# Kernel optimization log

Hardware: AMD Instinct MI355X
Metric: run time of the kernel (lower is better)

## Reference

```python
import jax, jax.numpy as jnp
import numpy as np

N_LAYERS = 4
BN_EPS = 1e-5


def setup_inputs() -> dict:
    key = jax.random.key(0)
    ks = jax.random.split(key, 10)
    N, E, F, H = 50000, 600000, 128, 128
    x = jax.random.normal(ks[0], (N, F), dtype=jnp.float32)
    edge_index = jax.random.randint(ks[1], (2, E), 0, N, dtype=jnp.int64)
    s = 0.05  # small init to keep deep ReLU stack numerically tame
    return {
        "x": x,
        "edge_index": edge_index,
        # stacked params for the 4 GINConv MLPs (num_features == hidden)
        "conv_w1": jax.random.normal(ks[2], (N_LAYERS, F, H), dtype=jnp.float32) * s,
        "conv_b1": jnp.zeros((N_LAYERS, H), dtype=jnp.float32),
        "conv_gamma": jnp.ones((N_LAYERS, H), dtype=jnp.float32),
        "conv_beta": jnp.zeros((N_LAYERS, H), dtype=jnp.float32),
        "conv_w2": jax.random.normal(ks[3], (N_LAYERS, H, H), dtype=jnp.float32) * s,
        "conv_b2": jnp.zeros((N_LAYERS, H), dtype=jnp.float32),
        "fc1_w": jax.random.normal(ks[4], (H, H), dtype=jnp.float32) * s,
        "fc1_b": jnp.zeros((H,), dtype=jnp.float32),
        "fc2_w": jax.random.normal(ks[5], (H, 1), dtype=jnp.float32) * s,
        "fc2_b": jnp.zeros((1,), dtype=jnp.float32),
    }


def _batchnorm(h, gamma, beta):
    # training-mode BatchNorm1d: batch stats over the node axis, biased variance
    mean = jnp.mean(h, axis=0, keepdims=True)
    var = jnp.mean(jnp.square(h - mean), axis=0, keepdims=True)
    return (h - mean) * jax.lax.rsqrt(var + BN_EPS) * gamma + beta


def _gin_layer(x, src, dst, w1, b1, gamma, beta, w2, b2):
    n = x.shape[0]
    # GIN sum aggregation with eps=0: (1+eps)*x_i + sum_{j->i} x_j
    agg = x + jax.ops.segment_sum(x[src], dst, num_segments=n)
    h = jax.nn.relu(agg @ w1 + b1)
    h = _batchnorm(h, gamma, beta)
    return jax.nn.relu(h @ w2 + b2)


def reference(x, edge_index, conv_w1, conv_b1, conv_gamma, conv_beta,
              conv_w2, conv_b2, fc1_w, fc1_b, fc2_w, fc2_b):
    src, dst = edge_index[0], edge_index[1]
    h = x
    for l in range(N_LAYERS):
        h = _gin_layer(h, src, dst, conv_w1[l], conv_b1[l], conv_gamma[l],
                       conv_beta[l], conv_w2[l], conv_b2[l])
    h = jax.nn.relu(h @ fc1_w + fc1_b)
    return h @ fc2_w + fc2_b  # [N, 1]
```

## Files before the change

### kernel.cpp

```cpp
#include <hip/hip_runtime.h>

constexpr int FEAT = 128;

typedef __attribute__((ext_vector_type(8))) _Float16 f16x8;
typedef __attribute__((ext_vector_type(4))) float f32x4;

__device__ inline unsigned int halfpair(float a, float b) {
  unsigned short ua = __builtin_bit_cast(unsigned short, (_Float16)a);
  unsigned short ub = __builtin_bit_cast(unsigned short, (_Float16)b);
  return (unsigned int)ua | ((unsigned int)ub << 16);
}
__device__ inline unsigned short halfr(float a) {
  return __builtin_bit_cast(unsigned short, (_Float16)a);
}
__device__ inline float2 halfup(unsigned int u) {
  _Float16 lo = __builtin_bit_cast(_Float16, (unsigned short)(u & 0xffffu));
  _Float16 hi = __builtin_bit_cast(_Float16, (unsigned short)(u >> 16));
  return make_float2((float)lo, (float)hi);
}

__device__ __host__ inline int kperm(int k) {
  return ((k >> 5) << 5) + (((k >> 2) & 3) << 3) + (((k >> 4) & 1) << 2) + (k & 3);
}


__global__ void count_kernel(const int* __restrict__ dst, int* __restrict__ deg, int E) {
  int e = blockIdx.x * blockDim.x + threadIdx.x;
  if (e < E) atomicAdd(&deg[dst[e]], 1);
}

__global__ __launch_bounds__(256) void scan1_kernel(const int* __restrict__ in,
                                                    int* __restrict__ bsum, int n) {
  int base = blockIdx.x * 1024 + threadIdx.x * 4;
  int s = 0;
  if (base + 3 < n) {
    int4 v = *(const int4*)(in + base);
    s = v.x + v.y + v.z + v.w;
  } else {
#pragma unroll
    for (int j = 0; j < 4; j++)
      if (base + j < n) s += in[base + j];
  }
#pragma unroll
  for (int off = 1; off < 64; off <<= 1) s += __shfl_xor(s, off);
  __shared__ int ws[4];
  int lane = threadIdx.x & 63, wid = threadIdx.x >> 6;
  if (lane == 0) ws[wid] = s;
  __syncthreads();
  if (threadIdx.x == 0) bsum[blockIdx.x] = ws[0] + ws[1] + ws[2] + ws[3];
}

__global__ __launch_bounds__(64) void scan2_kernel(int* __restrict__ bsum, int nb) {
  int t = threadIdx.x;
  int v = (t < nb) ? bsum[t] : 0;
  int s = v;
#pragma unroll
  for (int off = 1; off < 64; off <<= 1) {
    int u = __shfl_up(s, off);
    if (t >= off) s += u;
  }
  if (t < nb) bsum[t] = s - v;
}

__global__ __launch_bounds__(256) void scan3_kernel(const int* __restrict__ in,
                                                    const int* __restrict__ boff,
                                                    int* __restrict__ out,
                                                    int* __restrict__ out2, int n) {
  int t = threadIdx.x;
  int base = blockIdx.x * 1024 + t * 4;
  int v0 = 0, v1 = 0, v2 = 0, v3 = 0;
  if (base + 3 < n) {
    int4 v = *(const int4*)(in + base);
    v0 = v.x; v1 = v.y; v2 = v.z; v3 = v.w;
  } else {
    if (base + 0 < n) v0 = in[base + 0];
    if (base + 1 < n) v1 = in[base + 1];
    if (base + 2 < n) v2 = in[base + 2];
  }
  int ts = v0 + v1 + v2 + v3;
  int s = ts;
  int lane = t & 63, wid = t >> 6;
#pragma unroll
  for (int off = 1; off < 64; off <<= 1) {
    int u = __shfl_up(s, off);
    if (lane >= off) s += u;
  }
  __shared__ int ws[4];
  if (lane == 63) ws[wid] = s;
  __syncthreads();
  int cross = 0;
#pragma unroll
  for (int i = 0; i < 4; i++)
    if (i < wid) cross += ws[i];
  int excl = boff[blockIdx.x] + cross + (s - ts);
  int o0 = excl, o1 = o0 + v0, o2 = o1 + v1, o3 = o2 + v2;
  if (base + 3 < n) {
    *(int4*)(out + base) = make_int4(o0, o1, o2, o3);
    *(int4*)(out2 + base) = make_int4(o0, o1, o2, o3);
  } else {
    if (base + 0 < n) { out[base + 0] = o0; out2[base + 0] = o0; }
    if (base + 1 < n) { out[base + 1] = o1; out2[base + 1] = o1; }
    if (base + 2 < n) { out[base + 2] = o2; out2[base + 2] = o2; }
  }
}

__global__ void fill_kernel(const int* __restrict__ src, const int* __restrict__ dst,
                            int* __restrict__ cursor, int* __restrict__ col, int E) {
  int e = blockIdx.x * blockDim.x + threadIdx.x;
  if (e < E) {
    int p = atomicAdd(&cursor[dst[e]], 1);
    col[p] = src[e];
  }
}


__global__ void convert_kernel(const float* __restrict__ x, unsigned short* __restrict__ xb,
                               int n4) {
  int idx = blockIdx.x * blockDim.x + threadIdx.x;
  if (idx >= n4) return;
  float4 v = ((const float4*)x)[idx];
  uint2 o;
  o.x = halfpair(v.x, v.y);
  o.y = halfpair(v.z, v.w);
  ((uint2*)xb)[idx] = o;
}


__global__ void wconv_kernel(const float* __restrict__ w1, const float* __restrict__ fc1w,
                             unsigned short* __restrict__ dst) {
  int idx = blockIdx.x * blockDim.x + threadIdx.x;
  if (idx >= 5 * FEAT * FEAT) return;
  int m = idx >> 14;
  int r = idx & (FEAT * FEAT - 1);
  int k = r >> 7, n = r & 127;
  float v = (m < 4) ? w1[idx] : fc1w[r];
  int p = kperm(k);
  int slot = p >> 3, e = p & 7;
  dst[m * FEAT * FEAT + n * FEAT + ((slot ^ (n & 7)) << 3) + e] = halfr(v);
}


__global__ void agg_kernel(const unsigned short* __restrict__ x, const int* __restrict__ rowptr,
                           const int* __restrict__ col, unsigned short* __restrict__ agg, int N) {
  int gid = blockIdx.x * blockDim.x + threadIdx.x;
  int wid = gid >> 6;
  int lane = threadIdx.x & 63;
  int node = wid * 4 + (lane >> 4);
  if (node >= N) return;
  int ln = lane & 15;
  const uint4* xr = (const uint4*)x;
  uint4 s = xr[(size_t)node * 16 + ln];
  float2 t0 = halfup(s.x), t1 = halfup(s.y), t2 = halfup(s.z), t3 = halfup(s.w);
  float a0 = t0.x, a1 = t0.y, a2 = t1.x, a3 = t1.y;
  float a4 = t2.x, a5 = t2.y, a6 = t3.x, a7 = t3.y;
  float b0 = 0.f, b1 = 0.f, b2 = 0.f, b3 = 0.f;
  float b4 = 0.f, b5 = 0.f, b6 = 0.f, b7 = 0.f;
  int e0 = rowptr[node], e1 = rowptr[node + 1];
  int e = e0;
  for (; e + 3 < e1; e += 4) {
    int c0 = col[e], c1 = col[e + 1], c2 = col[e + 2], c3 = col[e + 3];
    uint4 v = xr[(size_t)c0 * 16 + ln];
    uint4 u = xr[(size_t)c1 * 16 + ln];
    uint4 w = xr[(size_t)c2 * 16 + ln];
    uint4 z = xr[(size_t)c3 * 16 + ln];
    float2 f;
    f = halfup(v.x); a0 += f.x; a1 += f.y;
    f = halfup(v.y); a2 += f.x; a3 += f.y;
    f = halfup(v.z); a4 += f.x; a5 += f.y;
    f = halfup(v.w); a6 += f.x; a7 += f.y;
    f = halfup(u.x); b0 += f.x; b1 += f.y;
    f = halfup(u.y); b2 += f.x; b3 += f.y;
    f = halfup(u.z); b4 += f.x; b5 += f.y;
    f = halfup(u.w); b6 += f.x; b7 += f.y;
    f = halfup(w.x); a0 += f.x; a1 += f.y;
    f = halfup(w.y); a2 += f.x; a3 += f.y;
    f = halfup(w.z); a4 += f.x; a5 += f.y;
    f = halfup(w.w); a6 += f.x; a7 += f.y;
    f = halfup(z.x); b0 += f.x; b1 += f.y;
    f = halfup(z.y); b2 += f.x; b3 += f.y;
    f = halfup(z.z); b4 += f.x; b5 += f.y;
    f = halfup(z.w); b6 += f.x; b7 += f.y;
  }
  for (; e < e1; e++) {
    uint4 v = xr[(size_t)col[e] * 16 + ln];
    float2 f;
    f = halfup(v.x); a0 += f.x; a1 += f.y;
    f = halfup(v.y); a2 += f.x; a3 += f.y;
    f = halfup(v.z); a4 += f.x; a5 += f.y;
    f = halfup(v.w); a6 += f.x; a7 += f.y;
  }
  a0 += b0; a1 += b1; a2 += b2; a3 += b3;
  a4 += b4; a5 += b5; a6 += b6; a7 += b7;
  uint4 o;
  o.x = halfpair(a0, a1);
  o.y = halfpair(a2, a3);
  o.z = halfpair(a4, a5);
  o.w = halfpair(a6, a7);
  ((uint4*)agg)[(size_t)node * 16 + ln] = o;
}


__global__ __launch_bounds__(512, 4) void gemm_kernel(
    const unsigned short* __restrict__ A, const unsigned short* __restrict__ Wimg,
    const float* __restrict__ bias, unsigned short* __restrict__ C,
    float* __restrict__ pS, float* __restrict__ pQ, int N, int mode,
    const float* __restrict__ fc2w, const float* __restrict__ fc2b,
    float* __restrict__ outp) {
  __shared__ unsigned short Al[FEAT * FEAT];
  __shared__ unsigned short Wl[FEAT * FEAT];
  __shared__ float ls[FEAT], lq[FEAT];

  int tx = threadIdx.x;
  int row0 = blockIdx.x * FEAT;
  if (tx < FEAT) { ls[tx] = 0.f; lq[tx] = 0.f; }

#pragma unroll
  for (int i = 0; i < 4; i++) {
    int idx = tx + i * 512;
    ((uint4*)Wl)[idx] = ((const uint4*)Wimg)[idx];
  }
#pragma unroll
  for (int i = 0; i < 8; i++) {
    int idx = tx + i * 512;
    int r = idx >> 5;
    int c = idx & 31;
    uint2 v = make_uint2(0u, 0u);
    if (row0 + r < N) v = ((const uint2*)(A + (size_t)(row0 + r) * FEAT))[c];
    int k0 = c << 2;
    int p0 = ((k0 >> 5) << 5) + (((k0 >> 2) & 3) << 3) + (((k0 >> 4) & 1) << 2);
    int slot = p0 >> 3, half4 = (p0 >> 2) & 1;
    *(uint2*)&Al[r * FEAT + ((slot ^ (r & 7)) << 3) + (half4 << 2)] = v;
  }
  __syncthreads();

  int w = tx >> 6;
  int l = tx & 63;
  int llo = l & 15, lhi = l >> 4;
  int wr = (w >> 2) * 64;
  int wc = (w & 3) * 32;

  f32x4 acc[4][2];
#pragma unroll
  for (int mi = 0; mi < 4; mi++)
#pragma unroll
    for (int nj = 0; nj < 2; nj++) acc[mi][nj] = (f32x4)(0.f);

#pragma unroll
  for (int s = 0; s < 4; s++) {
    f16x8 af[4], wf[2];
#pragma unroll
    for (int mi = 0; mi < 4; mi++) {
      int row = wr + mi * 16 + llo;
      af[mi] = *(const f16x8*)&Al[row * FEAT + ((((s << 2) + lhi) ^ (row & 7)) << 3)];
    }
#pragma unroll
    for (int nj = 0; nj < 2; nj++) {
      int n = wc + nj * 16 + llo;
      wf[nj] = *(const f16x8*)&Wl[n * FEAT + ((((s << 2) + lhi) ^ (n & 7)) << 3)];
    }
#pragma unroll
    for (int mi = 0; mi < 4; mi++)
#pragma unroll
      for (int nj = 0; nj < 2; nj++)
        acc[mi][nj] = __builtin_amdgcn_mfma_f32_16x16x32_f16(wf[nj], af[mi], acc[mi][nj], 0, 0, 0);
  }

  if (mode == 2) {
    float* red = ls;
    float pr[4] = {0.f, 0.f, 0.f, 0.f};
#pragma unroll
    for (int nj = 0; nj < 2; nj++) {
      int colb = wc + nj * 16 + lhi * 4;
      float4 bb = *(const float4*)&bias[colb];
      float4 fw = *(const float4*)&fc2w[colb];
#pragma unroll
      for (int mi = 0; mi < 4; mi++) {
        f32x4 v = acc[mi][nj];
        float v0 = fmaxf(v[0] + bb.x, 0.f);
        float v1 = fmaxf(v[1] + bb.y, 0.f);
        float v2 = fmaxf(v[2] + bb.z, 0.f);
        float v3 = fmaxf(v[3] + bb.w, 0.f);
        pr[mi] += v0 * fw.x + v1 * fw.y + v2 * fw.z + v3 * fw.w;
      }
    }
#pragma unroll
    for (int mi = 0; mi < 4; mi++) {
      float r = pr[mi];
      r += __shfl_xor(r, 16);
      r += __shfl_xor(r, 32);
      if (lhi == 0) atomicAdd(&red[wr + mi * 16 + llo], r);
    }
    __syncthreads();
    if (tx < FEAT) {
      int row = row0 + tx;
      if (row < N) outp[row] = red[tx] + fc2b[0];
    }
    return;
  }

#pragma unroll
  for (int nj = 0; nj < 2; nj++) {
    int colb = wc + nj * 16 + lhi * 4;
    float4 bb = *(const float4*)&bias[colb];
    float ps[4] = {0.f, 0.f, 0.f, 0.f}, pq[4] = {0.f, 0.f, 0.f, 0.f};
#pragma unroll
    for (int mi = 0; mi < 4; mi++) {
      int row = row0 + wr + mi * 16 + llo;
      f32x4 v = acc[mi][nj];
      float v0 = fmaxf(v[0] + bb.x, 0.f);
      float v1 = fmaxf(v[1] + bb.y, 0.f);
      float v2 = fmaxf(v[2] + bb.z, 0.f);
      float v3 = fmaxf(v[3] + bb.w, 0.f);
      if (row < N) {
        *(uint2*)&C[(size_t)row * FEAT + colb] = make_uint2(halfpair(v0, v1), halfpair(v2, v3));
        ps[0] += v0; ps[1] += v1; ps[2] += v2; ps[3] += v3;
        pq[0] += v0 * v0; pq[1] += v1 * v1; pq[2] += v2 * v2; pq[3] += v3 * v3;
      }
    }
    if (mode == 1) {
#pragma unroll
      for (int r = 0; r < 4; r++) {
        float s2 = ps[r], q2 = pq[r];
#pragma unroll
        for (int off = 1; off < 16; off <<= 1) {
          s2 += __shfl_xor(s2, off);
          q2 += __shfl_xor(q2, off);
        }
        if (llo == 0) {
          atomicAdd(&ls[colb + r], s2);
          atomicAdd(&lq[colb + r], q2);
        }
      }
    }
  }
  if (mode == 1) {
    __syncthreads();
    if (tx < FEAT) {
      pS[(size_t)blockIdx.x * FEAT + tx] = ls[tx];
      pQ[(size_t)blockIdx.x * FEAT + tx] = lq[tx];
    }
  }
}


__global__ __launch_bounds__(64) void stats_kernel(
    const float* __restrict__ pS, const float* __restrict__ pQ, int nblk,
    const float* __restrict__ gamma, const float* __restrict__ beta,
    float* __restrict__ scf, float* __restrict__ shf, int N) {
  int c = blockIdx.x;
  int ln = threadIdx.x;
  float s = 0.f, q = 0.f;
  for (int b = ln; b < nblk; b += 64) {
    s += pS[(size_t)b * FEAT + c];
    q += pQ[(size_t)b * FEAT + c];
  }
#pragma unroll
  for (int off = 32; off; off >>= 1) {
    s += __shfl_xor(s, off);
    q += __shfl_xor(q, off);
  }
  if (ln == 0) {
    float invN = 1.0f / (float)N;
    float mean = s * invN;
    float var = q * invN - mean * mean;
    float rstd = rsqrtf(var + 1e-5f);
    float scale = gamma[c] * rstd;
    scf[c] = scale;
    shf[c] = beta[c] - mean * scale;
  }
}


__global__ __launch_bounds__(128) void fold2_kernel(
    const float* __restrict__ scf, const float* __restrict__ shf,
    const float* __restrict__ w2, const float* __restrict__ b2,
    unsigned short* __restrict__ w2f, float* __restrict__ b2f) {
  __shared__ float red[FEAT];
  int c = blockIdx.x;
  int k = threadIdx.x;
  float wv = w2[k * FEAT + c];
  int p = kperm(k);
  int slot = p >> 3, e = p & 7;
  w2f[c * FEAT + ((slot ^ (c & 7)) << 3) + e] = halfr(scf[k] * wv);
  red[k] = shf[k] * wv;
  __syncthreads();
#pragma unroll
  for (int off = 64; off > 0; off >>= 1) {
    if (k < off) red[k] += red[k + off];
    __syncthreads();
  }
  if (k == 0) b2f[c] = b2[c] + red[0];
}


extern "C" void kernel_launch(void* const* d_in, const int* in_sizes, int n_in,
                              void* d_out, int out_size, void* d_ws, size_t ws_size,
                              hipStream_t stream) {
  const float* x     = (const float*)d_in[0];
  const int*   ei    = (const int*)d_in[1];
  const float* w1    = (const float*)d_in[2];
  const float* b1    = (const float*)d_in[3];
  const float* gamma = (const float*)d_in[4];
  const float* beta  = (const float*)d_in[5];
  const float* w2    = (const float*)d_in[6];
  const float* b2    = (const float*)d_in[7];
  const float* fc1w  = (const float*)d_in[8];
  const float* fc1b  = (const float*)d_in[9];
  const float* fc2w  = (const float*)d_in[10];
  const float* fc2b  = (const float*)d_in[11];
  float* out = (float*)d_out;

  int N = in_sizes[0] / FEAT;
  int E = in_sizes[1] / 2;
  const int* srcI = ei;
  const int* dstI = ei + E;

  int gemmBlocks = (N + FEAT - 1) / FEAT;
  int n = N + 1;
  int nb = (n + 1023) / 1024;

  size_t Nf = (size_t)N * FEAT;
  unsigned short* H = (unsigned short*)d_ws;
  unsigned short* G = H + Nf;
  unsigned short* wimg = G + Nf;
  unsigned short* w2f = wimg + 5 * FEAT * FEAT;
  float* b2f = (float*)(w2f + FEAT * FEAT);
  float* scf = b2f + FEAT;
  float* shf = scf + FEAT;
  float* pS = shf + FEAT;
  float* pQ = pS + (size_t)gemmBlocks * FEAT;
  int* deg = (int*)(pQ + (size_t)gemmBlocks * FEAT);
  int* rowptr = deg + ((n + 3) & ~3);
  int* cursor = rowptr + ((n + 3) & ~3);
  int* bsum = cursor + ((n + 3) & ~3);
  int* col = bsum + 64;

  hipMemsetAsync(deg, 0, n * sizeof(int), stream);
  count_kernel<<<(E + 255) / 256, 256, 0, stream>>>(dstI, deg, E);
  scan1_kernel<<<nb, 256, 0, stream>>>(deg, bsum, n);
  scan2_kernel<<<1, 64, 0, stream>>>(bsum, nb);
  scan3_kernel<<<nb, 256, 0, stream>>>(deg, bsum, rowptr, cursor, n);
  fill_kernel<<<(E + 255) / 256, 256, 0, stream>>>(srcI, dstI, cursor, col, E);

  int n4 = (int)(Nf / 4);
  convert_kernel<<<(n4 + 255) / 256, 256, 0, stream>>>(x, H, n4);
  wconv_kernel<<<(5 * FEAT * FEAT + 255) / 256, 256, 0, stream>>>(w1, fc1w, wimg);

  int aggBlocks = (int)((((size_t)(N + 3) / 4) * 64 + 255) / 256);

  for (int l = 0; l < 4; l++) {
    agg_kernel<<<aggBlocks, 256, 0, stream>>>(H, rowptr, col, G, N);
    gemm_kernel<<<gemmBlocks, 512, 0, stream>>>(
        G, wimg + (size_t)l * FEAT * FEAT, b1 + (size_t)l * FEAT, G, pS, pQ, N, 1,
        nullptr, nullptr, nullptr);
    stats_kernel<<<FEAT, 64, 0, stream>>>(pS, pQ, gemmBlocks, gamma + (size_t)l * FEAT,
                                          beta + (size_t)l * FEAT, scf, shf, N);
    fold2_kernel<<<FEAT, FEAT, 0, stream>>>(scf, shf, w2 + (size_t)l * FEAT * FEAT,
                                            b2 + (size_t)l * FEAT, w2f, b2f);
    gemm_kernel<<<gemmBlocks, 512, 0, stream>>>(
        G, w2f, b2f, H, nullptr, nullptr, N, 0, nullptr, nullptr, nullptr);
  }

  gemm_kernel<<<gemmBlocks, 512, 0, stream>>>(
      H, wimg + (size_t)4 * FEAT * FEAT, fc1b, nullptr, nullptr, nullptr, N, 2,
      fc2w, fc2b, out);
}
```

Baseline: 393.3 us.

## Fuse prep kernels and read GEMM weight fragments directly from global memory

Merges the degree count, input fp16 conversion and weight-image conversion into one launch using block-range dispatch, which removes two kernel launches. In the GEMM, the weight tile is no longer staged in LDS; each wave loads its W fragments straight from global/L2, halving shared memory per block. The A-tile staging now uses 16-byte global loads instead of 8-byte ones. The trade-off is that the weight fragments, which are identical for every block, are fetched repeatedly from cache instead of once into LDS, while the smaller LDS footprint may allow more blocks per CU.

```diff
diff --git a/kernel.cpp b/kernel.cpp
--- a/kernel.cpp
+++ b/kernel.cpp
@@ -24,10 +24,38 @@
 }
 
 
-__global__ void count_kernel(const int* __restrict__ dst, int* __restrict__ deg, int E) {
-  int e = blockIdx.x * blockDim.x + threadIdx.x;
-  if (e < E) atomicAdd(&deg[dst[e]], 1);
-}
+__global__ __launch_bounds__(256) void prep_kernel(
+    const float* __restrict__ x, unsigned short* __restrict__ xb, int n4,
+    const float* __restrict__ w1, const float* __restrict__ fc1w,
+    unsigned short* __restrict__ wimg,
+    const int* __restrict__ dst, int* __restrict__ deg, int E, int B1, int B2) {
+  int bid = blockIdx.x;
+  if (bid < B1) {
+    int idx = bid * 256 + threadIdx.x;
+    if (idx < n4) {
+      float4 v = ((const float4*)x)[idx];
+      uint2 o;
+      o.x = halfpair(v.x, v.y);
+      o.y = halfpair(v.z, v.w);
+      ((uint2*)xb)[idx] = o;
+    }
+  } else if (bid < B1 + B2) {
+    int idx = (bid - B1) * 256 + threadIdx.x;
+    if (idx < 5 * FEAT * FEAT) {
+      int m = idx >> 14;
+      int r = idx & (FEAT * FEAT - 1);
+      int k = r >> 7, n = r & 127;
+      float v = (m < 4) ? w1[idx] : fc1w[r];
+      int p = kperm(k);
+      int slot = p >> 3, e = p & 7;
+      wimg[m * FEAT * FEAT + n * FEAT + ((slot ^ (n & 7)) << 3) + e] = halfr(v);
+    }
+  } else {
+    int e = (bid - B1 - B2) * 256 + threadIdx.x;
+    if (e < E) atomicAdd(&deg[dst[e]], 1);
+  }
+}
+
 
 __global__ __launch_bounds__(256) void scan1_kernel(const int* __restrict__ in,
                                                     int* __restrict__ bsum, int n) {
@@ -111,32 +139,6 @@
     int p = atomicAdd(&cursor[dst[e]], 1);
     col[p] = src[e];
   }
-}
-
-
-__global__ void convert_kernel(const float* __restrict__ x, unsigned short* __restrict__ xb,
-                               int n4) {
-  int idx = blockIdx.x * blockDim.x + threadIdx.x;
-  if (idx >= n4) return;
-  float4 v = ((const float4*)x)[idx];
-  uint2 o;
-  o.x = halfpair(v.x, v.y);
-  o.y = halfpair(v.z, v.w);
-  ((uint2*)xb)[idx] = o;
-}
-
-
-__global__ void wconv_kernel(const float* __restrict__ w1, const float* __restrict__ fc1w,
-                             unsigned short* __restrict__ dst) {
-  int idx = blockIdx.x * blockDim.x + threadIdx.x;
-  if (idx >= 5 * FEAT * FEAT) return;
-  int m = idx >> 14;
-  int r = idx & (FEAT * FEAT - 1);
-  int k = r >> 7, n = r & 127;
-  float v = (m < 4) ? w1[idx] : fc1w[r];
-  int p = kperm(k);
-  int slot = p >> 3, e = p & 7;
-  dst[m * FEAT * FEAT + n * FEAT + ((slot ^ (n & 7)) << 3) + e] = halfr(v);
 }
 
 
@@ -207,7 +209,6 @@
     const float* __restrict__ fc2w, const float* __restrict__ fc2b,
     float* __restrict__ outp) {
   __shared__ unsigned short Al[FEAT * FEAT];
-  __shared__ unsigned short Wl[FEAT * FEAT];
   __shared__ float ls[FEAT], lq[FEAT];
 
   int tx = threadIdx.x;
@@ -217,19 +218,16 @@
 #pragma unroll
   for (int i = 0; i < 4; i++) {
     int idx = tx + i * 512;
-    ((uint4*)Wl)[idx] = ((const uint4*)Wimg)[idx];
-  }
-#pragma unroll
-  for (int i = 0; i < 8; i++) {
-    int idx = tx + i * 512;
-    int r = idx >> 5;
-    int c = idx & 31;
-    uint2 v = make_uint2(0u, 0u);
-    if (row0 + r < N) v = ((const uint2*)(A + (size_t)(row0 + r) * FEAT))[c];
-    int k0 = c << 2;
-    int p0 = ((k0 >> 5) << 5) + (((k0 >> 2) & 3) << 3) + (((k0 >> 4) & 1) << 2);
-    int slot = p0 >> 3, half4 = (p0 >> 2) & 1;
-    *(uint2*)&Al[r * FEAT + ((slot ^ (r & 7)) << 3) + (half4 << 2)] = v;
+    int r = idx >> 4;
+    int c = idx & 15;
+    uint4 v = make_uint4(0u, 0u, 0u, 0u);
+    if (row0 + r < N) v = ((const uint4*)(A + (size_t)(row0 + r) * FEAT))[c];
+    int k0 = c << 3;
+    int slotA = ((k0 >> 5) << 2) + ((k0 >> 2) & 3);
+    int sub = (k0 >> 4) & 1;
+    int sw = r & 7;
+    *(uint2*)&Al[r * FEAT + ((slotA ^ sw) << 3) + (sub << 2)] = make_uint2(v.x, v.y);
+    *(uint2*)&Al[r * FEAT + (((slotA + 1) ^ sw) << 3) + (sub << 2)] = make_uint2(v.z, v.w);
   }
   __syncthreads();
 
@@ -239,6 +237,9 @@
   int wr = (w >> 2) * 64;
   int wc = (w & 3) * 32;
 
+  const unsigned short* w0p = Wimg + (size_t)(wc + llo) * FEAT;
+  int m0 = (wc + llo) & 7;
+
   f32x4 acc[4][2];
 #pragma unroll
   for (int mi = 0; mi < 4; mi++)
@@ -247,22 +248,21 @@
 
 #pragma unroll
   for (int s = 0; s < 4; s++) {
-    f16x8 af[4], wf[2];
+    int so = (s << 2) + lhi;
+    int woff = (so ^ m0) << 3;
+    f16x8 wf0 = *(const f16x8*)&w0p[woff];
+    f16x8 wf1 = *(const f16x8*)&w0p[16 * FEAT + woff];
+    f16x8 af[4];
 #pragma unroll
     for (int mi = 0; mi < 4; mi++) {
       int row = wr + mi * 16 + llo;
-      af[mi] = *(const f16x8*)&Al[row * FEAT + ((((s << 2) + lhi) ^ (row & 7)) << 3)];
-    }
-#pragma unroll
-    for (int nj = 0; nj < 2; nj++) {
-      int n = wc + nj * 16 + llo;
-      wf[nj] = *(const f16x8*)&Wl[n * FEAT + ((((s << 2) + lhi) ^ (n & 7)) << 3)];
-    }
-#pragma unroll
-    for (int mi = 0; mi < 4; mi++)
-#pragma unroll
-      for (int nj = 0; nj < 2; nj++)
-        acc[mi][nj] = __builtin_amdgcn_mfma_f32_16x16x32_f16(wf[nj], af[mi], acc[mi][nj], 0, 0, 0);
+      af[mi] = *(const f16x8*)&Al[row * FEAT + ((so ^ (row & 7)) << 3)];
+    }
+#pragma unroll
+    for (int mi = 0; mi < 4; mi++) {
+      acc[mi][0] = __builtin_amdgcn_mfma_f32_16x16x32_f16(wf0, af[mi], acc[mi][0], 0, 0, 0);
+      acc[mi][1] = __builtin_amdgcn_mfma_f32_16x16x32_f16(wf1, af[mi], acc[mi][1], 0, 0, 0);
+    }
   }
 
   if (mode == 2) {
@@ -436,15 +436,16 @@
   int* col = bsum + 64;
 
   hipMemsetAsync(deg, 0, n * sizeof(int), stream);
-  count_kernel<<<(E + 255) / 256, 256, 0, stream>>>(dstI, deg, E);
+  int n4 = (int)(Nf / 4);
+  int B1 = (n4 + 255) / 256;
+  int B2 = (5 * FEAT * FEAT + 255) / 256;
+  int B3 = (E + 255) / 256;
+  prep_kernel<<<B1 + B2 + B3, 256, 0, stream>>>(x, H, n4, w1, fc1w, wimg, dstI, deg, E, B1, B2);
+
   scan1_kernel<<<nb, 256, 0, stream>>>(deg, bsum, n);
   scan2_kernel<<<1, 64, 0, stream>>>(bsum, nb);
   scan3_kernel<<<nb, 256, 0, stream>>>(deg, bsum, rowptr, cursor, n);
-  fill_kernel<<<(E + 255) / 256, 256, 0, stream>>>(srcI, dstI, cursor, col, E);
-
-  int n4 = (int)(Nf / 4);
-  convert_kernel<<<(n4 + 255) / 256, 256, 0, stream>>>(x, H, n4);
-  wconv_kernel<<<(5 * FEAT * FEAT + 255) / 256, 256, 0, stream>>>(w1, fc1w, wimg);
+  fill_kernel<<<B3, 256, 0, stream>>>(srcI, dstI, cursor, col, E);
 
   int aggBlocks = (int)((((size_t)(N + 3) / 4) * 64 + 255) / 256);
 
```

Result: no change. 386.3 us (-1.8%).
